# Optimization experiments

Measured on AMD Instinct MI355X. Metric: run time of the kernel, lower is better.

The kernel has to match this reference:

```python
import jax, jax.numpy as jnp
import numpy as np

B, T, S, E, H, D = 4, 1024, 1024, 1024, 16, 64


def _ln(x, g, b, eps=1e-5):
    m = x.mean(-1, keepdims=True)
    v = ((x - m) ** 2).mean(-1, keepdims=True)
    return (x - m) * jax.lax.rsqrt(v + eps) * g + b


def _mha(xq, xkv, mask4, Wq, Wk, Wv, Wo, bo):
    # Wq/Wk/Wv: [H, E, D] (stacked per-head bias-free linears)
    q = jnp.einsum('bte,hed->bhtd', xq, Wq)
    k = jnp.einsum('bse,hed->bhsd', xkv, Wk)
    v = jnp.einsum('bse,hed->bhsd', xkv, Wv)
    # NOTE: original scales by C**-0.5 with C = n_embd, not head_size
    wei = jnp.einsum('bhtd,bhsd->bhts', q, k) * (float(E) ** -0.5)
    wei = jnp.where(mask4 == 0, jnp.float32(-1e9), wei)
    wei = jax.nn.softmax(wei, axis=-1)
    o = jnp.einsum('bhts,bhsd->bhtd', wei, v)  # [B,H,T,D]
    b_, h_, t_, d_ = o.shape
    o = o.transpose(0, 2, 1, 3).reshape(b_, t_, h_ * d_)
    return o @ Wo + bo


def setup_inputs() -> dict:
    key = jax.random.key(0)
    ks = jax.random.split(key, 24)
    sd = 0.02
    inp = {
        'x': jax.random.normal(ks[0], (B, T, E), jnp.float32),
        'x_m': jnp.ones((B, 1, T), jnp.int32),
        'ca': jax.random.normal(ks[1], (B, S, E), jnp.float32),
        'ca_m': jnp.ones((B, 1, S), jnp.int32),
        'Wq_s': jax.random.normal(ks[2], (H, E, D), jnp.float32) * sd,
        'Wk_s': jax.random.normal(ks[3], (H, E, D), jnp.float32) * sd,
        'Wv_s': jax.random.normal(ks[4], (H, E, D), jnp.float32) * sd,
        'Wo_s': jax.random.normal(ks[5], (E, E), jnp.float32) * sd,
        'bo_s': jnp.zeros((E,), jnp.float32),
        'Wq_c': jax.random.normal(ks[6], (H, E, D), jnp.float32) * sd,
        'Wk_c': jax.random.normal(ks[7], (H, E, D), jnp.float32) * sd,
        'Wv_c': jax.random.normal(ks[8], (H, E, D), jnp.float32) * sd,
        'Wo_c': jax.random.normal(ks[9], (E, E), jnp.float32) * sd,
        'bo_c': jnp.zeros((E,), jnp.float32),
        'ln1_g': jnp.ones((E,), jnp.float32), 'ln1_b': jnp.zeros((E,), jnp.float32),
        'ln2_g': jnp.ones((E,), jnp.float32), 'ln2_b': jnp.zeros((E,), jnp.float32),
        'ln3_g': jnp.ones((E,), jnp.float32), 'ln3_b': jnp.zeros((E,), jnp.float32),
        'W1': jax.random.normal(ks[10], (E, 4 * E), jnp.float32) * sd,
        'b1': jnp.zeros((4 * E,), jnp.float32),
        'W2': jax.random.normal(ks[11], (4 * E, E), jnp.float32) * sd,
        'b2': jnp.zeros((E,), jnp.float32),
    }
    return inp


def reference(x, x_m, ca, ca_m, Wq_s, Wk_s, Wv_s, Wo_s, bo_s,
              Wq_c, Wk_c, Wv_c, Wo_c, bo_c,
              ln1_g, ln1_b, ln2_g, ln2_b, ln3_g, ln3_b,
              W1, b1, W2, b2):
    tril = jnp.tril(jnp.ones((T, T), jnp.int32))
    # self-attn mask: x_m [B,1,T] & tril [T,T] -> [B,1,T,T] (broadcast over heads)
    self_mask = x_m[:, :, None, :] * tril          # [B,1,T,T]
    cross_mask = ca_m[:, :, None, :]               # [B,1,1,S]
    x = x + _mha(_ln(x, ln1_g, ln1_b), _ln(x, ln1_g, ln1_b) if False else _ln(x, ln1_g, ln1_b), self_mask, Wq_s, Wk_s, Wv_s, Wo_s, bo_s)
    x = x + _mha(_ln(x, ln2_g, ln2_b), ca, cross_mask, Wq_c, Wk_c, Wv_c, Wo_c, bo_c)
    h = _ln(x, ln3_g, ln3_b)
    x = x + (jax.nn.relu(h @ W1 + b1) @ W2 + b2)
    return x
```

## Files before the change

kernel.cpp:

```cpp
#include <hip/hip_runtime.h>
#include <hip/hip_bf16.h>
#include <cstdint>
#include <cstddef>

typedef __attribute__((ext_vector_type(8))) short  s8v;
typedef __attribute__((ext_vector_type(4))) short  s4v;
typedef __attribute__((ext_vector_type(8))) __bf16 b8v;
typedef __attribute__((ext_vector_type(4))) float  f32x4;
typedef __attribute__((ext_vector_type(4))) unsigned u32x4;

#define SC2Q 0.0450843293f

__device__ __forceinline__ short f2bf(float f){
  unsigned u = __builtin_bit_cast(unsigned, f);
  unsigned r = (u + 0x7fffu + ((u >> 16) & 1u)) >> 16;
  return (short)(unsigned short)r;
}
__device__ __forceinline__ float bf2f(short s){
  return __builtin_bit_cast(float, ((unsigned)(unsigned short)s) << 16);
}

__device__ __forceinline__ f32x4 mfma16(s8v a, s8v b, f32x4 c){
  return __builtin_amdgcn_mfma_f32_16x16x32_bf16(
      __builtin_bit_cast(b8v, a), __builtin_bit_cast(b8v, b), c, 0, 0, 0);
}

__device__ __forceinline__ unsigned cvtpk(float a, float b){
  unsigned w;
  asm("v_cvt_pk_bf16_f32 %0, %1, %2" : "=v"(w) : "v"(a), "v"(b));
  return w;
}

__global__ __launch_bounds__(256)
void ln_k(const float* __restrict__ x, const float* __restrict__ g,
          const float* __restrict__ b, short* __restrict__ out)
{
  const int row = blockIdx.x, tid = threadIdx.x;
  const float4 v = ((const float4*)(x + (size_t)row*1024))[tid];
  float s  = v.x+v.y+v.z+v.w;
  float s2 = v.x*v.x+v.y*v.y+v.z*v.z+v.w*v.w;
  #pragma unroll
  for (int off=32; off; off>>=1){ s += __shfl_down(s, off); s2 += __shfl_down(s2, off); }
  __shared__ float red[8];
  const int wave = tid>>6, lane = tid&63;
  if (lane==0){ red[wave]=s; red[4+wave]=s2; }
  __syncthreads();
  s  = red[0]+red[1]+red[2]+red[3];
  s2 = red[4]+red[5]+red[6]+red[7];
  const float mean = s*(1.f/1024.f);
  const float rstd = rsqrtf(s2*(1.f/1024.f) - mean*mean + 1e-5f);
  const float4 gv = ((const float4*)g)[tid];
  const float4 bv = ((const float4*)b)[tid];
  s4v o;
  o[0] = f2bf((v.x-mean)*rstd*gv.x + bv.x);
  o[1] = f2bf((v.y-mean)*rstd*gv.y + bv.y);
  o[2] = f2bf((v.z-mean)*rstd*gv.z + bv.z);
  o[3] = f2bf((v.w-mean)*rstd*gv.w + bv.w);
  *(s4v*)(out + (size_t)row*1024 + tid*4) = o;
}

__global__ __launch_bounds__(256)
void cast_k(const float* __restrict__ in, short* __restrict__ out)
{
  const int i = blockIdx.x*256 + threadIdx.x;
  const float4 v = ((const float4*)in)[i];
  s4v o; o[0]=f2bf(v.x); o[1]=f2bf(v.y); o[2]=f2bf(v.z); o[3]=f2bf(v.w);
  ((s4v*)out)[i] = o;
}

__global__ __launch_bounds__(256)
void mkb_k(const int* __restrict__ xm, const int* __restrict__ cm,
           float* __restrict__ mbS, float* __restrict__ mbC)
{
  const int i = blockIdx.x*256 + threadIdx.x;
  mbS[i] = xm[i] ? 0.f : -1.5e9f;
  mbC[i] = cm[i] ? 0.f : -1.5e9f;
}

__global__ __launch_bounds__(256)
void tcast_k(const float* __restrict__ in, short* __restrict__ out, int E2, int D2)
{
  __shared__ float t[32][33];
  const int h  = blockIdx.z;
  const int e0 = blockIdx.x*32, d0 = blockIdx.y*32;
  const int tx = threadIdx.x & 31, ty = threadIdx.x >> 5;
  const float* ip = in + (size_t)h*E2*D2;
  #pragma unroll
  for (int r = ty; r < 32; r += 8)
    t[r][tx] = ip[(size_t)(e0+r)*D2 + d0 + tx];
  __syncthreads();
  short* op = out + (size_t)h*D2*E2;
  #pragma unroll
  for (int r = ty; r < 32; r += 8)
    op[(size_t)(d0+r)*E2 + e0 + tx] = f2bf(t[tx][r]);
}

__global__ __launch_bounds__(256)
void vtrans_k(const short* __restrict__ V, int ldv, short* __restrict__ Vt, int S, int H)
{
  __shared__ short t[32][34];
  const int bh = blockIdx.z;
  const int b = bh / H, h = bh % H;
  const int s0 = blockIdx.x*32, d0 = blockIdx.y*32;
  const int tx = threadIdx.x & 31, ty = threadIdx.x >> 5;
  const short* ip = V + (size_t)b*S*ldv + h*64;
  #pragma unroll
  for (int r = ty; r < 32; r += 8)
    t[r][tx] = ip[(size_t)(s0+r)*ldv + d0 + tx];
  __syncthreads();
  const int s  = s0 + tx;
  const int ks = (s>>5)&1, bb = (tx>>4)&1, hh = (tx>>2)&3, rr = tx&3;
  const int cp = (s & ~63) + ks*32 + hh*8 + bb*4 + rr;
  short* op = Vt + ((size_t)bh*64 + d0)*S;
  #pragma unroll
  for (int r = ty; r < 32; r += 8)
    op[(size_t)r*S + cp] = t[tx][r];
}

__global__ __launch_bounds__(256)
void red4_k(const short* __restrict__ p, const float* __restrict__ bias,
            const float* __restrict__ resid, float* __restrict__ out)
{
  const int i = blockIdx.x*256 + threadIdx.x;
  float4 o = ((const float4*)resid)[i];
  const float4 bv = ((const float4*)bias)[i & 255];
  o.x += bv.x; o.y += bv.y; o.z += bv.z; o.w += bv.w;
  #pragma unroll
  for (int z=0; z<4; z++){
    const s4v v = ((const s4v*)(p + (size_t)z*4194304))[i];
    o.x += bf2f(v[0]); o.y += bf2f(v[1]); o.z += bf2f(v[2]); o.w += bf2f(v[3]);
  }
  ((float4*)out)[i] = o;
}

template<int BN, int BIAS, int RELU, int RESID, int WF32, int SCQ>
__global__ __launch_bounds__(256, 2)
void gemm_bt(const short* __restrict__ A, const short* __restrict__ Bt,
             const float* __restrict__ bias, const float* __restrict__ resid,
             short* __restrict__ Cb, float* __restrict__ Cf,
             int M, int N, int K)
{
  __shared__ short lds[3][128*32 + BN*32];
  const int nwg = gridDim.x * gridDim.y;
  int id = blockIdx.y * gridDim.x + blockIdx.x;
  id = (id & 7) * (nwg >> 3) + (id >> 3);
  const int bx = id % gridDim.x, by = id / gridDim.x;
  const int m0 = by*128, n0 = bx*BN;

  const int tid  = threadIdx.x;
  const int wave = tid>>6, lane = tid&63;
  const int lo = lane&15, hi = lane>>4;
  const int wm = wave>>1, wn = wave&1;

  constexpr int NJ = BN/32;
  constexpr int BC = BN>>6;
  f32x4 acc[4][NJ] = {};
  const int NK = K >> 5;

  auto stage = [&](int buf, int kt){
    const short* Ag = A  + (size_t)m0*K + kt*32;
    const short* Bg = Bt + (size_t)n0*K + kt*32;
    #pragma unroll
    for (int c=0;c<2;c++){
      const int q = (wave*2+c)*64 + lane;
      const int r = q>>2, cc = q&3;
      __builtin_amdgcn_global_load_lds(
        (const __attribute__((address_space(1))) void*)(Ag + (size_t)r*K + cc*8),
        (__attribute__((address_space(3))) void*)(&lds[buf][(wave*2+c)*512]),
        16, 0, 0);
    }
    #pragma unroll
    for (int c=0;c<BC;c++){
      const int q = (wave*BC+c)*64 + lane;
      const int r = q>>2, cc = q&3;
      __builtin_amdgcn_global_load_lds(
        (const __attribute__((address_space(1))) void*)(Bg + (size_t)r*K + cc*8),
        (__attribute__((address_space(3))) void*)(&lds[buf][4096 + (wave*BC+c)*512]),
        16, 0, 0);
    }
  };

  stage(0, 0);
  if (NK > 1) stage(1, 1);

  for (int kt=0; kt<NK; kt++){
    if (kt+1 < NK){
      if constexpr (BN==128) asm volatile("s_waitcnt vmcnt(4)" ::: "memory");
      else                   asm volatile("s_waitcnt vmcnt(3)" ::: "memory");
    } else {
      asm volatile("s_waitcnt vmcnt(0)" ::: "memory");
    }
    __builtin_amdgcn_s_barrier();
    __builtin_amdgcn_sched_barrier(0);
    if (kt+2 < NK) stage((kt+2)%3, kt+2);

    const short* la = &lds[kt%3][0];
    const short* lb = &lds[kt%3][4096];
    s8v af[4], bfr[NJ];
    #pragma unroll
    for (int i=0;i<4;i++)
      af[i] = *(const s8v*)(la + (wm*64 + i*16 + lo)*32 + hi*8);
    #pragma unroll
    for (int j=0;j<NJ;j++)
      bfr[j] = *(const s8v*)(lb + (wn*(BN/2) + j*16 + lo)*32 + hi*8);
    #pragma unroll
    for (int i=0;i<4;i++)
      #pragma unroll
      for (int j=0;j<NJ;j++)
        acc[i][j] = mfma16(af[i], bfr[j], acc[i][j]);
  }

  #pragma unroll
  for (int i=0;i<4;i++){
    const int row = m0 + wm*64 + i*16 + hi*4;
    #pragma unroll
    for (int j=0;j<NJ;j++){
      const int col = n0 + wn*(BN/2) + j*16 + lo;
      const float bv = BIAS ? bias[col] : 0.0f;
      #pragma unroll
      for (int r=0;r<4;r++){
        float v = acc[i][j][r] + bv;
        if constexpr (SCQ==2) v *= SC2Q;
        if (RELU) v = fmaxf(v, 0.0f);
        const size_t idx = (size_t)(row + r)*N + col;
        if (RESID) v += resid[idx];
        if (WF32) Cf[idx] = v; else Cb[idx] = f2bf(v);
      }
    }
  }
}

template<int BIAS, int RELU, int RESID, int WF32, int SCQ>
__global__ __launch_bounds__(512, 1)
void gemm256(const short* __restrict__ A, int lda,
             const short* __restrict__ Bt, int ldb,
             const float* __restrict__ bias, const float* __restrict__ resid,
             short* __restrict__ Cb, float* __restrict__ Cf,
             int M, int N, int K)
{
  __shared__ short lds[2][32768];
  const int nwg = gridDim.x * gridDim.y;
  int id = blockIdx.y * gridDim.x + blockIdx.x;
  id = (id & 7) * (nwg >> 3) + (id >> 3);
  const int bx = id % gridDim.x, by = id / gridDim.x;
  const int m0 = by*256, n0 = bx*256;
  A  += (size_t)blockIdx.z * K;
  Bt += (size_t)blockIdx.z * K;
  const size_t cofs = (size_t)blockIdx.z * M * N;

  const int tid = threadIdx.x;
  const int lane = tid&63, wave = tid>>6;
  const int lo = lane&15, hi = lane>>4;
  const int wr = wave>>2, wc = wave&3;

  f32x4 acc[8][4] = {};
  const int NT = K >> 6;

  auto stageA = [&](int buf, int kt, int part){
    const short* Ag = A + (size_t)m0*lda + kt*64;
    const int q = part*512 + tid;
    const int r = q>>3, c = q&7;
    __builtin_amdgcn_global_load_lds(
      (const __attribute__((address_space(1))) void*)(Ag + (size_t)r*lda + ((c^(r&7))*8)),
      (__attribute__((address_space(3))) void*)(&lds[buf][q*8]), 16, 0, 0);
  };
  auto stageB = [&](int buf, int kt, int part){
    const short* Bg = Bt + (size_t)n0*ldb + kt*64;
    const int q = part*512 + tid;
    const int r = q>>3, c = q&7;
    __builtin_amdgcn_global_load_lds(
      (const __attribute__((address_space(1))) void*)(Bg + (size_t)r*ldb + ((c^(r&7))*8)),
      (__attribute__((address_space(3))) void*)(&lds[buf][16384 + q*8]), 16, 0, 0);
  };

  #pragma unroll
  for (int p=0;p<4;p++){ stageA(0,0,p); stageB(0,0,p); }
  __syncthreads();

  for (int t=0; t<NT; t++){
    const int cur = t&1;
    const short* la = &lds[cur][0];
    const short* lb = &lds[cur][16384];
    const bool pf = (t+1 < NT);
    #pragma unroll
    for (int ks=0; ks<2; ks++){
      s8v bf[4];
      #pragma unroll
      for (int j=0;j<4;j++){
        const int r = wc*64 + j*16 + lo;
        bf[j] = *(const s8v*)(lb + r*64 + (((ks*4+hi)^(r&7))*8));
      }
      #pragma unroll
      for (int mh=0; mh<2; mh++){
        s8v af[4];
        #pragma unroll
        for (int i=0;i<4;i++){
          const int r = wr*128 + mh*64 + i*16 + lo;
          af[i] = *(const s8v*)(la + r*64 + (((ks*4+hi)^(r&7))*8));
        }
        if (pf && ks==0){
          stageA(cur^1, t+1, mh*2);   stageB(cur^1, t+1, mh*2);
          stageA(cur^1, t+1, mh*2+1); stageB(cur^1, t+1, mh*2+1);
        }
        __builtin_amdgcn_s_setprio(1);
        #pragma unroll
        for (int i=0;i<4;i++)
          #pragma unroll
          for (int j=0;j<4;j++)
            acc[mh*4+i][j] = mfma16(af[i], bf[j], acc[mh*4+i][j]);
        __builtin_amdgcn_s_setprio(0);
      }
    }
    __syncthreads();
  }

  #pragma unroll
  for (int I=0;I<8;I++){
    const int row = m0 + wr*128 + I*16 + hi*4;
    #pragma unroll
    for (int j=0;j<4;j++){
      const int col = n0 + wc*64 + j*16 + lo;
      const float bv = BIAS ? bias[col] : 0.0f;
      #pragma unroll
      for (int r=0;r<4;r++){
        float v = acc[I][j][r] + bv;
        if constexpr (SCQ==1) { if (col < 1024) v *= SC2Q; }
        if (RELU) v = fmaxf(v, 0.0f);
        const size_t idx = cofs + (size_t)(row + r)*N + col;
        if (RESID) v += resid[idx];
        if (WF32) Cf[idx] = v; else Cb[idx] = f2bf(v);
      }
    }
  }
}

template<int CAUSAL>
__global__ __launch_bounds__(256, 4)
void attn_k(const short* __restrict__ Q, int ldq,
            const short* __restrict__ K, int ldk,
            const short* __restrict__ Vt, int ldvt,
            const float* __restrict__ mbias,
            short* __restrict__ O, int ldo,
            int H, int Tq, int Sk)
{
  __shared__ short kls[2][4096];
  __shared__ short vls[2][4096];
  const int bh = blockIdx.x;
  const int b = bh / H, h = bh % H;
  const int tid = threadIdx.x;
  const int wave = tid>>6, lane = tid&63;
  const int lo = lane&15, hi = lane>>4;
  const int t0 = blockIdx.y*64 + wave*16;

  const short* Qb  = Q + (size_t)(b*Tq)*ldq + h*64;
  const short* Kb  = K + (size_t)(b*Sk)*ldk + h*64;
  const short* Vtb = Vt + (size_t)bh*64*ldvt;

  const short* qp = Qb + (size_t)(t0+lo)*ldq + hi*8;
  const s8v qa0 = *(const s8v*)(qp);
  const s8v qa1 = *(const s8v*)(qp + 32);

  float mrow = -INFINITY;
  f32x4 oacc[4] = {};
  f32x4 oaccL = {};
  const int trow = t0 + lo;
  const int nblk = CAUSAL ? (blockIdx.y + 1) : (Sk>>6);
  const int x8 = lo & 7;

  const s8v onesv = {(short)0x3F80,(short)0x3F80,(short)0x3F80,(short)0x3F80,
                     (short)0x3F80,(short)0x3F80,(short)0x3F80,(short)0x3F80};

  const int q0 = tid, q1 = 256 + tid;
  const int r0 = q0>>3, cs0 = ((q0&7) ^ (r0&7))*8;
  const int r1 = q1>>3, cs1 = ((q1&7) ^ (r1&7))*8;
  const short* kS0 = Kb + (size_t)r0*ldk + cs0;
  const short* kS1 = Kb + (size_t)r1*ldk + cs1;
  const short* vS0 = Vtb + (size_t)r0*ldvt + cs0;
  const short* vS1 = Vtb + (size_t)r1*ldvt + cs1;
  const size_t kAdv = (size_t)64*ldk;

  auto stage = [&](int buf){
    __builtin_amdgcn_global_load_lds(
      (const __attribute__((address_space(1))) void*)kS0,
      (__attribute__((address_space(3))) void*)(&kls[buf][wave*512]), 16, 0, 0);
    __builtin_amdgcn_global_load_lds(
      (const __attribute__((address_space(1))) void*)kS1,
      (__attribute__((address_space(3))) void*)(&kls[buf][2048 + wave*512]), 16, 0, 0);
    __builtin_amdgcn_global_load_lds(
      (const __attribute__((address_space(1))) void*)vS0,
      (__attribute__((address_space(3))) void*)(&vls[buf][wave*512]), 16, 0, 0);
    __builtin_amdgcn_global_load_lds(
      (const __attribute__((address_space(1))) void*)vS1,
      (__attribute__((address_space(3))) void*)(&vls[buf][2048 + wave*512]), 16, 0, 0);
    kS0 += kAdv; kS1 += kAdv; vS0 += 64; vS1 += 64;
  };

  const char* klsB = (const char*)kls;
  const char* vlsB = (const char*)vls;
  const int A0 = lo*128 + ((hi     ^ x8)*16);
  const int A1 = lo*128 + (((4+hi) ^ x8)*16);
  int curB = 0;

  const char* mbp = (const char*)(mbias + (size_t)b*Sk) + hi*16;

  stage(0);
  for (int it=0; it<nblk; it++){
    __syncthreads();
    if (it+1 < nblk) stage((it+1)&1);

    const char* ka0 = klsB + curB + A0;
    const char* ka1 = klsB + curB + A1;
    s8v kf[4][2];
    #pragma unroll
    for (int g=0; g<4; g++){
      kf[g][0] = *(const s8v*)(ka0 + g*2048);
      kf[g][1] = *(const s8v*)(ka1 + g*2048);
    }

    f32x4 sg[4] = {};
    __builtin_amdgcn_s_setprio(1);
    #pragma unroll
    for (int g=0; g<4; g++){
      sg[g] = mfma16(kf[g][0], qa0, sg[g]);
      sg[g] = mfma16(kf[g][1], qa1, sg[g]);
    }
    __builtin_amdgcn_s_setprio(0);

    float p[4][4];
    #pragma unroll
    for (int g=0; g<4; g++){
      const f32x4 mv = *(const f32x4*)(mbp + g*64);
      #pragma unroll
      for (int r=0; r<4; r++)
        p[g][r] = sg[g][r] + mv[r];
    }
    mbp += 256;
    if (CAUSAL && it == nblk-1){
      const int s0 = it*64;
      #pragma unroll
      for (int g=0; g<4; g++)
        #pragma unroll
        for (int r=0; r<4; r++){
          const int sidx = s0 + g*16 + 4*hi + r;
          if (sidx > trow) p[g][r] = -1.5e9f;
        }
    }

    float bmax;
    {
      const float m0_ = fmaxf(fmaxf(p[0][0],p[0][1]),p[0][2]);
      const float m1_ = fmaxf(fmaxf(p[0][3],p[1][0]),p[1][1]);
      const float m2_ = fmaxf(fmaxf(p[1][2],p[1][3]),p[2][0]);
      const float m3_ = fmaxf(fmaxf(p[2][1],p[2][2]),p[2][3]);
      const float m4_ = fmaxf(fmaxf(p[3][0],p[3][1]),p[3][2]);
      bmax = fmaxf(fmaxf(fmaxf(m0_,m1_),m2_), fmaxf(fmaxf(m3_,m4_),p[3][3]));
    }
    bmax = fmaxf(bmax, __shfl_xor(bmax, 16));
    bmax = fmaxf(bmax, __shfl_xor(bmax, 32));

    if (!__all(bmax <= mrow + 8.0f)){
      const float mn  = fmaxf(mrow, bmax);
      const float fac = exp2f(mrow - mn);
      mrow = mn;
      #pragma unroll
      for (int f=0; f<4; f++)
        #pragma unroll
        for (int r=0; r<4; r++)
          oacc[f][r] *= fac;
      #pragma unroll
      for (int r=0; r<4; r++) oaccL[r] *= fac;
    }

    #pragma unroll
    for (int g=0; g<4; g++)
      #pragma unroll
      for (int r=0; r<4; r++)
        p[g][r] = exp2f(p[g][r] - mrow);

    u32x4 pw0, pw1;
    pw0[0] = cvtpk(p[0][0], p[0][1]);
    pw0[1] = cvtpk(p[0][2], p[0][3]);
    pw0[2] = cvtpk(p[1][0], p[1][1]);
    pw0[3] = cvtpk(p[1][2], p[1][3]);
    pw1[0] = cvtpk(p[2][0], p[2][1]);
    pw1[1] = cvtpk(p[2][2], p[2][3]);
    pw1[2] = cvtpk(p[3][0], p[3][1]);
    pw1[3] = cvtpk(p[3][2], p[3][3]);
    const s8v pb0 = __builtin_bit_cast(s8v, pw0);
    const s8v pb1 = __builtin_bit_cast(s8v, pw1);

    const char* va0 = vlsB + curB + A0;
    const char* va1 = vlsB + curB + A1;
    __builtin_amdgcn_s_setprio(1);
    #pragma unroll
    for (int f=0; f<4; f++){
      const s8v av0 = *(const s8v*)(va0 + f*2048);
      const s8v av1 = *(const s8v*)(va1 + f*2048);
      oacc[f] = mfma16(av0, pb0, oacc[f]);
      oacc[f] = mfma16(av1, pb1, oacc[f]);
    }
    oaccL = mfma16(onesv, pb0, oaccL);
    oaccL = mfma16(onesv, pb1, oaccL);
    __builtin_amdgcn_s_setprio(0);
    curB ^= 8192;
  }

  const float inv = 1.0f / oaccL[0];
  short* Ob = O + (size_t)(b*Tq)*ldo + h*64 + (size_t)(t0+lo)*ldo + 4*hi;
  #pragma unroll
  for (int f=0; f<4; f++){
    s4v o;
    #pragma unroll
    for (int r=0; r<4; r++) o[r] = f2bf(oacc[f][r]*inv);
    *(s4v*)(Ob + f*16) = o;
  }
}

extern "C" void kernel_launch(void* const* d_in, const int* in_sizes, int n_in,
                              void* d_out, int out_size, void* d_ws, size_t ws_size,
                              hipStream_t stream)
{
  (void)in_sizes; (void)n_in; (void)out_size; (void)ws_size;
  const float* x    = (const float*)d_in[0];
  const int*   xm   = (const int*)  d_in[1];
  const float* ca   = (const float*)d_in[2];
  const int*   cam  = (const int*)  d_in[3];
  const float* Wq_s = (const float*)d_in[4];
  const float* Wk_s = (const float*)d_in[5];
  const float* Wv_s = (const float*)d_in[6];
  const float* Wo_s = (const float*)d_in[7];
  const float* bo_s = (const float*)d_in[8];
  const float* Wq_c = (const float*)d_in[9];
  const float* Wk_c = (const float*)d_in[10];
  const float* Wv_c = (const float*)d_in[11];
  const float* Wo_c = (const float*)d_in[12];
  const float* bo_c = (const float*)d_in[13];
  const float* ln1g = (const float*)d_in[14];
  const float* ln1b = (const float*)d_in[15];
  const float* ln2g = (const float*)d_in[16];
  const float* ln2b = (const float*)d_in[17];
  const float* ln3g = (const float*)d_in[18];
  const float* ln3b = (const float*)d_in[19];
  const float* W1   = (const float*)d_in[20];
  const float* b1   = (const float*)d_in[21];
  const float* W2   = (const float*)d_in[22];
  const float* b2   = (const float*)d_in[23];
  float* out = (float*)d_out;

  char* ws = (char*)d_ws;
  size_t off = 0;
  auto alloc = [&](size_t bytes)->void*{
    void* p = ws + off; off += (bytes + 255) & ~(size_t)255; return p; };

  short* w_qkv_s = (short*)alloc((size_t)3072*1024*2);
  short* w_o_s   = (short*)alloc((size_t)1024*1024*2);
  short* w_q_c   = (short*)alloc((size_t)1024*1024*2);
  short* w_kv_c  = (short*)alloc((size_t)2048*1024*2);
  short* w_o_c   = (short*)alloc((size_t)1024*1024*2);
  short* w_1     = (short*)alloc((size_t)4096*1024*2);
  short* w_2     = (short*)alloc((size_t)1024*4096*2);
  short* xn      = (short*)alloc((size_t)4096*1024*2);
  short* cab     = (short*)alloc((size_t)4096*1024*2);
  short* qkv     = (short*)alloc((size_t)4096*3072*2);
  short* attno   = (short*)alloc((size_t)4096*1024*2);
  float* xres    = (float*)alloc((size_t)4096*1024*4);
  short* hffn    = (short*)alloc((size_t)4096*4096*2);
  float* pA      = (float*)alloc((size_t)4096*1024*4);
  float* pB      = (float*)alloc((size_t)4096*1024*4);
  float* mbS     = (float*)alloc((size_t)4096*4);
  float* mbC     = (float*)alloc((size_t)4096*4);
  short* pP      = (short*)pA;
  short* kvbuf   = qkv + (size_t)4096*1024;
  short* vt_s    = hffn;
  short* vt_c    = hffn + (size_t)4*1024*1024;
  (void)pB;

  tcast_k<<<dim3(32,  2,16),256,0,stream>>>(Wq_s, w_qkv_s,           1024,   64);
  tcast_k<<<dim3(32,  2,16),256,0,stream>>>(Wk_s, w_qkv_s+1024*1024, 1024,   64);
  tcast_k<<<dim3(32,  2,16),256,0,stream>>>(Wv_s, w_qkv_s+2048*1024, 1024,   64);
  tcast_k<<<dim3(32, 32, 1),256,0,stream>>>(Wo_s, w_o_s,             1024, 1024);
  tcast_k<<<dim3(32,  2,16),256,0,stream>>>(Wq_c, w_q_c,             1024,   64);
  tcast_k<<<dim3(32,  2,16),256,0,stream>>>(Wk_c, w_kv_c,            1024,   64);
  tcast_k<<<dim3(32,  2,16),256,0,stream>>>(Wv_c, w_kv_c+1024*1024,  1024,   64);
  tcast_k<<<dim3(32, 32, 1),256,0,stream>>>(Wo_c, w_o_c,             1024, 1024);
  tcast_k<<<dim3(32,128, 1),256,0,stream>>>(W1,   w_1,               1024, 4096);
  tcast_k<<<dim3(128,32, 1),256,0,stream>>>(W2,   w_2,               4096, 1024);
  cast_k<<<4096,256,0,stream>>>(ca, cab);
  mkb_k<<<16,256,0,stream>>>(xm, cam, mbS, mbC);

  ln_k<<<4096,256,0,stream>>>(x, ln1g, ln1b, xn);
  gemm256<0,0,0,0,1><<<dim3(12,16),512,0,stream>>>(xn, 1024, w_qkv_s, 1024,
                                                   nullptr, nullptr, qkv, nullptr,
                                                   4096, 3072, 1024);
  vtrans_k<<<dim3(32,2,64),256,0,stream>>>(qkv+2048, 3072, vt_s, 1024, 16);
  attn_k<1><<<dim3(64,16),256,0,stream>>>(qkv, 3072, qkv+1024, 3072, vt_s, 1024,
                                          mbS, attno, 1024, 16, 1024, 1024);
  gemm_bt<64,1,0,1,1,0><<<dim3(16,32),256,0,stream>>>(attno, w_o_s, bo_s, x,
                                                      nullptr, xres, 4096, 1024, 1024);

  ln_k<<<4096,256,0,stream>>>(xres, ln2g, ln2b, xn);
  gemm_bt<64,0,0,0,0,2><<<dim3(16,32),256,0,stream>>>(xn, w_q_c, nullptr, nullptr,
                                                      qkv, nullptr, 4096, 1024, 1024);
  gemm256<0,0,0,0,0><<<dim3(8,16),512,0,stream>>>(cab, 1024, w_kv_c, 1024,
                                                  nullptr, nullptr, kvbuf, nullptr,
                                                  4096, 2048, 1024);
  vtrans_k<<<dim3(32,2,64),256,0,stream>>>(kvbuf+1024, 2048, vt_c, 1024, 16);
  attn_k<0><<<dim3(64,16),256,0,stream>>>(qkv, 1024, kvbuf, 2048, vt_c, 1024,
                                          mbC, attno, 1024, 16, 1024, 1024);
  gemm_bt<64,1,0,1,1,0><<<dim3(16,32),256,0,stream>>>(attno, w_o_c, bo_c, xres,
                                                      nullptr, xres, 4096, 1024, 1024);

  ln_k<<<4096,256,0,stream>>>(xres, ln3g, ln3b, xn);
  gemm256<1,1,0,0,0><<<dim3(16,16),512,0,stream>>>(xn, 1024, w_1, 1024,
                                                   b1, nullptr, hffn, nullptr,
                                                   4096, 4096, 1024);
  gemm256<0,0,0,0,0><<<dim3(4,16,4),512,0,stream>>>(hffn, 4096, w_2, 4096,
                                                    nullptr, nullptr, pP, nullptr,
                                                    4096, 1024, 1024);
  red4_k<<<4096,256,0,stream>>>(pP, b2, xres, out);
}
```

Before: 362.4 us.

## Triple-buffer K/V in attention and software-pipeline QK^T with softmax/PV

Changes the attention kernel's K/V LDS staging from double to triple buffering, with two tiles in flight and explicit vmcnt waits plus raw s_barrier in place of __syncthreads. It also software-pipelines the loop so the QK^T MFMAs for the next tile are issued before the PV MFMAs of the current tile, ping-ponging score registers. The intent is to hide global-load latency and overlap softmax VALU work with matrix work. In exchange it uses more LDS and lowers the occupancy hint from 4 to 3 blocks per CU, and the hand-written waitcnt counts must stay correct.

```diff
diff --git a/kernel.cpp b/kernel.cpp
--- a/kernel.cpp
+++ b/kernel.cpp
@@ -335,7 +335,7 @@
 }
 
 template<int CAUSAL>
-__global__ __launch_bounds__(256, 4)
+__global__ __launch_bounds__(256, 3)
 void attn_k(const short* __restrict__ Q, int ldq,
             const short* __restrict__ K, int ldk,
             const short* __restrict__ Vt, int ldvt,
@@ -343,8 +343,8 @@
             short* __restrict__ O, int ldo,
             int H, int Tq, int Sk)
 {
-  __shared__ short kls[2][4096];
-  __shared__ short vls[2][4096];
+  __shared__ short kls[3][4096];
+  __shared__ short vls[3][4096];
   const int bh = blockIdx.x;
   const int b = bh / H, h = bh % H;
   const int tid = threadIdx.x;
@@ -379,19 +379,19 @@
   const short* vS1 = Vtb + (size_t)r1*ldvt + cs1;
   const size_t kAdv = (size_t)64*ldk;
 
-  auto stage = [&](int buf){
+  auto stage = [&](int b3){
     __builtin_amdgcn_global_load_lds(
       (const __attribute__((address_space(1))) void*)kS0,
-      (__attribute__((address_space(3))) void*)(&kls[buf][wave*512]), 16, 0, 0);
+      (__attribute__((address_space(3))) void*)(&kls[b3][wave*512]), 16, 0, 0);
     __builtin_amdgcn_global_load_lds(
       (const __attribute__((address_space(1))) void*)kS1,
-      (__attribute__((address_space(3))) void*)(&kls[buf][2048 + wave*512]), 16, 0, 0);
+      (__attribute__((address_space(3))) void*)(&kls[b3][2048 + wave*512]), 16, 0, 0);
     __builtin_amdgcn_global_load_lds(
       (const __attribute__((address_space(1))) void*)vS0,
-      (__attribute__((address_space(3))) void*)(&vls[buf][wave*512]), 16, 0, 0);
+      (__attribute__((address_space(3))) void*)(&vls[b3][wave*512]), 16, 0, 0);
     __builtin_amdgcn_global_load_lds(
       (const __attribute__((address_space(1))) void*)vS1,
-      (__attribute__((address_space(3))) void*)(&vls[buf][2048 + wave*512]), 16, 0, 0);
+      (__attribute__((address_space(3))) void*)(&vls[b3][2048 + wave*512]), 16, 0, 0);
     kS0 += kAdv; kS1 += kAdv; vS0 += 64; vS1 += 64;
   };
 
@@ -399,32 +399,34 @@
   const char* vlsB = (const char*)vls;
   const int A0 = lo*128 + ((hi     ^ x8)*16);
   const int A1 = lo*128 + (((4+hi) ^ x8)*16);
-  int curB = 0;
-
   const char* mbp = (const char*)(mbias + (size_t)b*Sk) + hi*16;
 
-  stage(0);
-  for (int it=0; it<nblk; it++){
-    __syncthreads();
-    if (it+1 < nblk) stage((it+1)&1);
-
-    const char* ka0 = klsB + curB + A0;
-    const char* ka1 = klsB + curB + A1;
-    s8v kf[4][2];
+  auto qk = [&](int b3, f32x4 (&sg)[4]){
+    const char* ka0 = klsB + b3*8192 + A0;
+    const char* ka1 = klsB + b3*8192 + A1;
+    s8v kf0[4], kf1[4];
     #pragma unroll
     for (int g=0; g<4; g++){
-      kf[g][0] = *(const s8v*)(ka0 + g*2048);
-      kf[g][1] = *(const s8v*)(ka1 + g*2048);
-    }
-
-    f32x4 sg[4] = {};
+      kf0[g] = *(const s8v*)(ka0 + g*2048);
+      kf1[g] = *(const s8v*)(ka1 + g*2048);
+    }
+    const f32x4 z = {};
     __builtin_amdgcn_s_setprio(1);
     #pragma unroll
     for (int g=0; g<4; g++){
-      sg[g] = mfma16(kf[g][0], qa0, sg[g]);
-      sg[g] = mfma16(kf[g][1], qa1, sg[g]);
+      sg[g] = mfma16(kf0[g], qa0, z);
+      sg[g] = mfma16(kf1[g], qa1, sg[g]);
     }
     __builtin_amdgcn_s_setprio(0);
+  };
+
+  f32x4 sgA[4], sgB[4];
+  int rB = 0, wB = 2;
+  auto nxt3 = [](int v){ return v==2 ? 0 : v+1; };
+
+  auto iter = [&](int t, f32x4 (&In)[4], f32x4 (&Out)[4]){
+    __builtin_amdgcn_s_barrier();
+    if (t+2 < nblk){ stage(wB); wB = nxt3(wB); }
 
     float p[4][4];
     #pragma unroll
@@ -432,11 +434,11 @@
       const f32x4 mv = *(const f32x4*)(mbp + g*64);
       #pragma unroll
       for (int r=0; r<4; r++)
-        p[g][r] = sg[g][r] + mv[r];
+        p[g][r] = In[g][r] + mv[r];
     }
     mbp += 256;
-    if (CAUSAL && it == nblk-1){
-      const int s0 = it*64;
+    if (CAUSAL && t == nblk-1){
+      const int s0 = t*64;
       #pragma unroll
       for (int g=0; g<4; g++)
         #pragma unroll
@@ -445,7 +447,6 @@
           if (sidx > trow) p[g][r] = -1.5e9f;
         }
     }
-
     float bmax;
     {
       const float m0_ = fmaxf(fmaxf(p[0][0],p[0][1]),p[0][2]);
@@ -457,7 +458,6 @@
     }
     bmax = fmaxf(bmax, __shfl_xor(bmax, 16));
     bmax = fmaxf(bmax, __shfl_xor(bmax, 32));
-
     if (!__all(bmax <= mrow + 8.0f)){
       const float mn  = fmaxf(mrow, bmax);
       const float fac = exp2f(mrow - mn);
@@ -470,7 +470,6 @@
       #pragma unroll
       for (int r=0; r<4; r++) oaccL[r] *= fac;
     }
-
     #pragma unroll
     for (int g=0; g<4; g++)
       #pragma unroll
@@ -489,8 +488,15 @@
     const s8v pb0 = __builtin_bit_cast(s8v, pw0);
     const s8v pb1 = __builtin_bit_cast(s8v, pw1);
 
-    const char* va0 = vlsB + curB + A0;
-    const char* va1 = vlsB + curB + A1;
+    if (t+1 < nblk){
+      if (t+2 < nblk) asm volatile("s_waitcnt vmcnt(4)" ::: "memory");
+      else            asm volatile("s_waitcnt vmcnt(0)" ::: "memory");
+    }
+    __builtin_amdgcn_s_barrier();
+    if (t+1 < nblk) qk(nxt3(rB), Out);
+
+    const char* va0 = vlsB + rB*8192 + A0;
+    const char* va1 = vlsB + rB*8192 + A1;
     __builtin_amdgcn_s_setprio(1);
     #pragma unroll
     for (int f=0; f<4; f++){
@@ -502,7 +508,19 @@
     oaccL = mfma16(onesv, pb0, oaccL);
     oaccL = mfma16(onesv, pb1, oaccL);
     __builtin_amdgcn_s_setprio(0);
-    curB ^= 8192;
+    rB = nxt3(rB);
+  };
+
+  stage(0); stage(1);
+  asm volatile("s_waitcnt vmcnt(4)" ::: "memory");
+  __builtin_amdgcn_s_barrier();
+  qk(0, sgA);
+
+  int t = 0;
+  while (t < nblk){
+    iter(t, sgA, sgB); t++;
+    if (t >= nblk) break;
+    iter(t, sgB, sgA); t++;
   }
 
   const float inv = 1.0f / oaccL[0];
```

After: 379.6 us. +4.8%, slower.
